# Optimization experiments

Measured on AMD Instinct MI355X. Metric: run time of the kernel, lower is better.

## Reference

```python
import jax, jax.numpy as jnp
import numpy as np

TAU = 2.0        # args.tau default (spikingjelly LIFNode)
V_TH = 1.0       # v_threshold
V_RESET = 0.0    # v_reset (hard reset)
ALPHA = 2.0      # ATan surrogate alpha

@jax.custom_vjp
def atan_spike(x):
    # Heaviside spike with ATan surrogate gradient (spikingjelly surrogate.ATan)
    return (x >= 0.0).astype(x.dtype)

def _atan_fwd(x):
    return atan_spike(x), x

def _atan_bwd(x, g):
    sg = (ALPHA / 2.0) / (1.0 + (jnp.pi / 2.0 * ALPHA * x) ** 2)
    return (g * sg,)

atan_spike.defvjp(_atan_fwd, _atan_bwd)

def setup_inputs() -> dict:
    key = jax.random.key(0)
    k1, k2, k3 = jax.random.split(key, 3)
    T, B, IN, OUT, NC = 16, 512, 3072, 2048, 10
    x_seq = jax.random.normal(k1, (T, B, IN), dtype=jnp.float32)
    # xavier-uniform-like scale: sqrt(2/(fan_in+fan_out))
    fc_w = jax.random.normal(k2, (OUT, IN), dtype=jnp.float32) * np.sqrt(2.0 / (IN + OUT)).astype(np.float32)
    fc_b = jnp.zeros((OUT,), jnp.float32)
    aux_w = jax.random.normal(k3, (NC, OUT), dtype=jnp.float32) * np.sqrt(2.0 / (OUT + NC)).astype(np.float32)
    aux_b = jnp.zeros((NC,), jnp.float32)
    return {"x_seq": x_seq, "fc_w": fc_w, "fc_b": fc_b, "aux_w": aux_w, "aux_b": aux_b}

def reference(x_seq, fc_w, fc_b, aux_w, aux_b):
    # fc over all timesteps: [T,B,in] @ [out,in]^T -> [T,B,out]
    cur_seq = jnp.einsum('tbi,oi->tbo', x_seq, fc_w) + fc_b

    def step(v, c):
        # LIF charge: v += (x - (v - v_reset)) / tau
        v = v + (c - (v - V_RESET)) / TAU
        s = atan_spike(v - V_TH)
        s_d = jax.lax.stop_gradient(s)  # detach_reset=True
        v = (1.0 - s_d) * v + s_d * V_RESET  # hard reset
        return v, s

    v0 = jnp.full(cur_seq.shape[1:], V_RESET, cur_seq.dtype)  # reset_net -> v = v_reset
    _, spk_seq = jax.lax.scan(step, v0, cur_seq)  # spk_seq: [T,B,out]
    count = spk_seq.sum(axis=0)                    # [B,out]
    logits = count @ aux_w.T + aux_b               # aux_head local logits [B,10]
    return spk_seq, count, logits
```

## Files before the change

kernel.cpp:

```cpp
#include <hip/hip_runtime.h>
#include <hip/hip_bf16.h>
#include <stdint.h>

#define T_   16
#define B_   512
#define IN_  3072
#define OUT_ 2048
#define NC_  10
#define M_   (T_ * B_)

#define BM 128
#define BN 128

#define SPK_SZ ((size_t)T_ * B_ * OUT_)
#define CNT_SZ ((size_t)B_ * OUT_)

#define TOL 4e-4
#define MAXFLAG (B_ * OUT_)

#define BK2   32
#define NCH2  (IN_ / BK2)
#define TILE_US 8192
#define APAN (M_ / BM)
#define BPAN (OUT_ / BN)

#define A_PREP_BLOCKS (APAN * NCH2 * 2)
#define B_PREP_BLOCKS (BPAN * NCH2 * 2)

typedef __attribute__((ext_vector_type(8))) short s16x8;
typedef __attribute__((ext_vector_type(4))) float f32x4;

__device__ unsigned int g_ctr;
__device__ unsigned int g_list[MAXFLAG];

__global__ void zero_ctr() { if (threadIdx.x == 0) g_ctr = 0; }

__device__ __forceinline__ unsigned short f2bf(float f) {
    __bf16 h = (__bf16)f;
    return *(unsigned short*)&h;
}
__device__ __forceinline__ float bf2f(unsigned short u) {
    union { unsigned int i; float f; } c; c.i = ((unsigned int)u) << 16; return c.f;
}
__device__ __forceinline__ int swz8(int r, int g) {
    return r * 64 + ((g ^ (r & 7)) << 3);
}

__device__ __forceinline__ void gload_lds16(const void* g, void* l) {
    __builtin_amdgcn_global_load_lds(
        (const __attribute__((address_space(1))) unsigned int*)g,
        (__attribute__((address_space(3))) unsigned int*)l, 16, 0, 0);
}

__global__ __launch_bounds__(256)
void prep2(const float* __restrict__ x, const float* __restrict__ w,
           unsigned short* __restrict__ Adig, unsigned short* __restrict__ Bdig)
{
    if (blockIdx.x == 0 && threadIdx.x == 0) g_ctr = 0;

    const float* src; unsigned short* dst; int id;
    if (blockIdx.x < A_PREP_BLOCKS) {
        src = x; dst = Adig; id = blockIdx.x * 256 + threadIdx.x;
    } else {
        src = w; dst = Bdig; id = (blockIdx.x - A_PREP_BLOCKS) * 256 + threadIdx.x;
    }
    const int gk = id & 3;
    const int r  = (id >> 2) & 127;
    const int ch = (id >> 9) % NCH2;
    const int pa = id / (NCH2 * 512);
    const int m  = pa * 128 + r;
    const int k  = ch * BK2 + gk * 8;

    float f[8];
    *(float4*)&f[0] = *(const float4*)(src + (size_t)m * IN_ + k);
    *(float4*)&f[4] = *(const float4*)(src + (size_t)m * IN_ + k + 4);
    s16x8 hi, lo;
#pragma unroll
    for (int j = 0; j < 8; ++j) {
        unsigned short hb = f2bf(f[j]);
        hi[j] = (short)hb;
        lo[j] = (short)f2bf(f[j] - bf2f(hb));
    }
    unsigned short* tb = dst + ((size_t)pa * NCH2 + ch) * TILE_US;
    *(s16x8*)&tb[swz8(r, gk)]     = hi;
    *(s16x8*)&tb[swz8(r, gk + 4)] = lo;
}

__global__ __launch_bounds__(256, 2)
void gemm_lds(const unsigned short* __restrict__ Adig,
              const unsigned short* __restrict__ Bdig,
              float* __restrict__ cur)
{
    __shared__ __align__(16) unsigned short Ash[2][TILE_US];
    __shared__ __align__(16) unsigned short Bsh[2][TILE_US];

    const int tid = threadIdx.x;
    const int l   = tid & 63;
    const int wv  = tid >> 6;
    const int wm  = (wv >> 1) * 64;
    const int wn  = (wv & 1) * 64;

    const int lin = blockIdx.x;
    const int xcd = lin & 7;
    const int jj  = lin >> 3;
    const int pm  = xcd * 8 + (jj & 7);
    const int pn  = jj >> 3;
    const int m0  = pm * BM;
    const int n0  = pn * BN;

    f32x4 acc[4][4];
#pragma unroll
    for (int i = 0; i < 4; ++i)
#pragma unroll
        for (int j = 0; j < 4; ++j) acc[i][j] = (f32x4)0.0f;

    const int lp = l & 15;
    const int lq = l >> 4;
    const int l8 = l * 8;

    const unsigned short* Abase = Adig + (size_t)pm * NCH2 * TILE_US;
    const unsigned short* Bbase = Bdig + (size_t)pn * NCH2 * TILE_US;

    auto stage = [&](int ch, int d) {
        if (wv < 2) {
            const unsigned short* sA = Abase + (size_t)ch * TILE_US + wv * 4096;
            unsigned short* dA = &Ash[d][wv * 4096];
#pragma unroll
            for (int i = 0; i < 8; ++i)
                gload_lds16(sA + i * 512 + l8, dA + i * 512);
        } else {
            const unsigned short* sB = Bbase + (size_t)ch * TILE_US + (wv - 2) * 4096;
            unsigned short* dB = &Bsh[d][(wv - 2) * 4096];
#pragma unroll
            for (int i = 0; i < 8; ++i)
                gload_lds16(sB + i * 512 + l8, dB + i * 512);
        }
    };

    stage(0, 0);

    for (int ch = 0; ch < NCH2; ++ch) {
        const int d = ch & 1;
        if (ch + 1 < NCH2) {
            stage(ch + 1, d ^ 1);
            asm volatile("s_waitcnt vmcnt(8)" ::: "memory");
        } else {
            asm volatile("s_waitcnt vmcnt(0)" ::: "memory");
        }
        __builtin_amdgcn_s_barrier();
        asm volatile("" ::: "memory");

        s16x8 a1f[4], a2f[4], b1f[4], b2f[4];
#pragma unroll
        for (int i = 0; i < 4; ++i) {
            const int ra = wm + i * 16 + lp;
            a1f[i] = *(const s16x8*)&Ash[d][swz8(ra, lq)];
            a2f[i] = *(const s16x8*)&Ash[d][swz8(ra, lq + 4)];
            const int rb = wn + i * 16 + lp;
            b1f[i] = *(const s16x8*)&Bsh[d][swz8(rb, lq)];
            b2f[i] = *(const s16x8*)&Bsh[d][swz8(rb, lq + 4)];
        }
        asm volatile("s_waitcnt lgkmcnt(0)" ::: "memory");
        __builtin_amdgcn_s_barrier();

        __builtin_amdgcn_s_setprio(1);
#pragma unroll
        for (int i = 0; i < 4; ++i)
#pragma unroll
            for (int j = 0; j < 4; ++j) {
                acc[i][j] = __builtin_amdgcn_mfma_f32_16x16x32_bf16(
                    a1f[i], b1f[j], acc[i][j], 0, 0, 0);
                acc[i][j] = __builtin_amdgcn_mfma_f32_16x16x32_bf16(
                    a2f[i], b1f[j], acc[i][j], 0, 0, 0);
                acc[i][j] = __builtin_amdgcn_mfma_f32_16x16x32_bf16(
                    a1f[i], b2f[j], acc[i][j], 0, 0, 0);
            }
        __builtin_amdgcn_s_setprio(0);
    }

    const int crow = lq * 4, ccol = lp;
#pragma unroll
    for (int i = 0; i < 4; ++i)
#pragma unroll
        for (int j = 0; j < 4; ++j) {
            const size_t mbase = (size_t)(m0 + wm + i * 16 + crow);
            const int o = n0 + wn + j * 16 + ccol;
#pragma unroll
            for (int reg = 0; reg < 4; ++reg)
                cur[(mbase + reg) * OUT_ + o] = acc[i][j][reg];
        }
}

__global__ __launch_bounds__(256, 2)
void gemm_split(const float* __restrict__ x, const float* __restrict__ w,
                float* __restrict__ cur)
{
    __shared__ __align__(16) unsigned short A1[BM * 64];
    __shared__ __align__(16) unsigned short A2[BM * 64];
    __shared__ __align__(16) unsigned short B1[BN * 64];
    __shared__ __align__(16) unsigned short B2[BN * 64];

    const int tid = threadIdx.x;
    const int l   = tid & 63;
    const int wv  = tid >> 6;
    const int wm  = (wv >> 1) * 64;
    const int wn  = (wv & 1) * 64;
    const int m0  = blockIdx.x * BM;
    const int n0  = blockIdx.y * BN;

    const int r = tid >> 1;
    const int h = tid & 1;
    const float* xa = x + (size_t)(m0 + r) * IN_ + h * 32;
    const float* wa = w + (size_t)(n0 + r) * IN_ + h * 32;

    f32x4 acc[4][4];
#pragma unroll
    for (int i = 0; i < 4; ++i)
#pragma unroll
        for (int j = 0; j < 4; ++j) acc[i][j] = (f32x4)0.0f;

    const int lp = l & 15;
    const int lq = l >> 4;

    for (int ch = 0; ch < 48; ++ch) {
        const int k0 = ch * 64;
        __syncthreads();
        float fx[32], fw[32];
#pragma unroll
        for (int i = 0; i < 8; ++i)
            *(float4*)&fx[4 * i] = *(const float4*)(xa + k0 + 4 * i);
#pragma unroll
        for (int i = 0; i < 8; ++i)
            *(float4*)&fw[4 * i] = *(const float4*)(wa + k0 + 4 * i);

#pragma unroll
        for (int q = 0; q < 4; ++q) {
            s16x8 vh, vl, uh, ul;
#pragma unroll
            for (int j = 0; j < 8; ++j) {
                float f = fx[8 * q + j];
                unsigned short hb = f2bf(f);
                vh[j] = (short)hb;
                vl[j] = (short)f2bf(f - bf2f(hb));
                float g = fw[8 * q + j];
                unsigned short gb = f2bf(g);
                uh[j] = (short)gb;
                ul[j] = (short)f2bf(g - bf2f(gb));
            }
            const int gg = h * 4 + q;
            *(s16x8*)&A1[swz8(r, gg)] = vh;
            *(s16x8*)&A2[swz8(r, gg)] = vl;
            *(s16x8*)&B1[swz8(r, gg)] = uh;
            *(s16x8*)&B2[swz8(r, gg)] = ul;
        }
        __syncthreads();

#pragma unroll
        for (int kk = 0; kk < 2; ++kk) {
            const int gb = kk * 4 + lq;
            s16x8 a1f[4], a2f[4], b1f[4], b2f[4];
#pragma unroll
            for (int i = 0; i < 4; ++i) {
                const int ra = wm + i * 16 + lp;
                a1f[i] = *(const s16x8*)&A1[swz8(ra, gb)];
                a2f[i] = *(const s16x8*)&A2[swz8(ra, gb)];
                const int rb = wn + i * 16 + lp;
                b1f[i] = *(const s16x8*)&B1[swz8(rb, gb)];
                b2f[i] = *(const s16x8*)&B2[swz8(rb, gb)];
            }
#pragma unroll
            for (int i = 0; i < 4; ++i)
#pragma unroll
                for (int j = 0; j < 4; ++j) {
                    acc[i][j] = __builtin_amdgcn_mfma_f32_16x16x32_bf16(
                        a1f[i], b1f[j], acc[i][j], 0, 0, 0);
                    acc[i][j] = __builtin_amdgcn_mfma_f32_16x16x32_bf16(
                        a2f[i], b1f[j], acc[i][j], 0, 0, 0);
                    acc[i][j] = __builtin_amdgcn_mfma_f32_16x16x32_bf16(
                        a1f[i], b2f[j], acc[i][j], 0, 0, 0);
                }
        }
    }

    const int crow = lq * 4, ccol = lp;
#pragma unroll
    for (int i = 0; i < 4; ++i)
#pragma unroll
        for (int j = 0; j < 4; ++j) {
            const size_t mbase = (size_t)(m0 + wm + i * 16 + crow);
            const int o = n0 + wn + j * 16 + ccol;
#pragma unroll
            for (int reg = 0; reg < 4; ++reg)
                cur[(mbase + reg) * OUT_ + o] = acc[i][j][reg];
        }
}

__global__ __launch_bounds__(256)
void lif_pass(const float* __restrict__ fcb, float* __restrict__ out)
{
    const int idx = blockIdx.x * 256 + threadIdx.x;
    const int o = idx & (OUT_ - 1);
    const double bias = (double)fcb[o];
    double v = 0.0; int cnt = 0; bool fl = false;
#pragma unroll
    for (int t = 0; t < T_; ++t) {
        const size_t p = (size_t)t * CNT_SZ + idx;
        double c = (double)out[p] + bias;
        v = v + (c - v) * 0.5;
        double d = v - 1.0;
        bool s = d >= 0.0;
        if (fabs(d) < TOL) fl = true;
        out[p] = s ? 1.0f : 0.0f;
        cnt += s ? 1 : 0;
        if (s) v = 0.0;
    }
    out[SPK_SZ + idx] = (float)cnt;
    if (fl) {
        unsigned int pI = atomicAdd(&g_ctr, 1u);
        g_list[pI] = (unsigned int)idx;
    }
}

__global__ void fixup(const float* __restrict__ x, const float* __restrict__ w,
                      const float* __restrict__ fcb, float* __restrict__ out)
{
    int nf = (int)g_ctr; if (nf > MAXFLAG) nf = MAXFLAG;
    const int lane = threadIdx.x & 63;
    const int wid  = (blockIdx.x * blockDim.x + threadIdx.x) >> 6;
    const int nw   = (gridDim.x * blockDim.x) >> 6;

    for (int i = wid; i < nf; i += nw) {
        unsigned int e = g_list[i];
        int b = (int)(e >> 11), o = (int)(e & (OUT_ - 1));
        double part[T_];
#pragma unroll
        for (int t = 0; t < T_; ++t) part[t] = 0.0;
        const float* wrow = w + (size_t)o * IN_;
        for (int k = lane; k < IN_; k += 64) {
            double wvv = (double)wrow[k];
#pragma unroll
            for (int t = 0; t < T_; ++t)
                part[t] = fma((double)x[((size_t)t * B_ + b) * IN_ + k], wvv, part[t]);
        }
#pragma unroll
        for (int t = 0; t < T_; ++t)
#pragma unroll
            for (int off = 32; off > 0; off >>= 1)
                part[t] += __shfl_xor(part[t], off, 64);
        if (lane == 0) {
            double bias = (double)fcb[o];
            double v = 0.0; int cnt = 0;
#pragma unroll
            for (int t = 0; t < T_; ++t) {
                double c = part[t] + bias;
                v = v + (c - v) * 0.5;
                bool s = (v - 1.0) >= 0.0;
                out[(size_t)t * CNT_SZ + (size_t)b * OUT_ + o] = s ? 1.0f : 0.0f;
                cnt += s ? 1 : 0;
                if (s) v = 0.0;
            }
            out[SPK_SZ + (size_t)b * OUT_ + o] = (float)cnt;
        }
    }
}

__global__ void aux_logits(const float* __restrict__ cnt,
                           const float* __restrict__ aw,
                           const float* __restrict__ ab,
                           float* __restrict__ lg)
{
    const int b = blockIdx.x;
    const int lane = threadIdx.x;
    double p0=0,p1=0,p2=0,p3=0,p4=0,p5=0,p6=0,p7=0,p8=0,p9=0;
    for (int o = lane; o < OUT_; o += 64) {
        double c = (double)cnt[(size_t)b * OUT_ + o];
        p0 = fma(c, (double)aw[0 * OUT_ + o], p0);
        p1 = fma(c, (double)aw[1 * OUT_ + o], p1);
        p2 = fma(c, (double)aw[2 * OUT_ + o], p2);
        p3 = fma(c, (double)aw[3 * OUT_ + o], p3);
        p4 = fma(c, (double)aw[4 * OUT_ + o], p4);
        p5 = fma(c, (double)aw[5 * OUT_ + o], p5);
        p6 = fma(c, (double)aw[6 * OUT_ + o], p6);
        p7 = fma(c, (double)aw[7 * OUT_ + o], p7);
        p8 = fma(c, (double)aw[8 * OUT_ + o], p8);
        p9 = fma(c, (double)aw[9 * OUT_ + o], p9);
    }
#pragma unroll
    for (int off = 32; off > 0; off >>= 1) {
        p0 += __shfl_xor(p0, off, 64); p1 += __shfl_xor(p1, off, 64);
        p2 += __shfl_xor(p2, off, 64); p3 += __shfl_xor(p3, off, 64);
        p4 += __shfl_xor(p4, off, 64); p5 += __shfl_xor(p5, off, 64);
        p6 += __shfl_xor(p6, off, 64); p7 += __shfl_xor(p7, off, 64);
        p8 += __shfl_xor(p8, off, 64); p9 += __shfl_xor(p9, off, 64);
    }
    if (lane == 0) {
        double pv[NC_] = {p0,p1,p2,p3,p4,p5,p6,p7,p8,p9};
#pragma unroll
        for (int c = 0; c < NC_; ++c)
            lg[(size_t)b * NC_ + c] = (float)(pv[c] + (double)ab[c]);
    }
}

extern "C" void kernel_launch(void* const* d_in, const int* in_sizes, int n_in,
                              void* d_out, int out_size, void* d_ws, size_t ws_size,
                              hipStream_t stream)
{
    (void)in_sizes; (void)n_in; (void)out_size;
    const float* x   = (const float*)d_in[0];
    const float* w   = (const float*)d_in[1];
    const float* fcb = (const float*)d_in[2];
    const float* aw  = (const float*)d_in[3];
    const float* ab  = (const float*)d_in[4];
    float* out = (float*)d_out;

    const size_t needA = (size_t)APAN * NCH2 * TILE_US * 2;
    const size_t needB = (size_t)BPAN * NCH2 * TILE_US * 2;

    if (ws_size >= needA + needB) {
        unsigned short* Adig = (unsigned short*)d_ws;
        unsigned short* Bdig = Adig + (size_t)APAN * NCH2 * TILE_US;
        prep2<<<dim3(A_PREP_BLOCKS + B_PREP_BLOCKS), dim3(256), 0, stream>>>(
            x, w, Adig, Bdig);
        gemm_lds<<<dim3(APAN * BPAN), dim3(256), 0, stream>>>(Adig, Bdig, out);
    } else {
        zero_ctr<<<dim3(1), dim3(64), 0, stream>>>();
        gemm_split<<<dim3(M_ / BM, OUT_ / BN), dim3(256), 0, stream>>>(x, w, out);
    }

    lif_pass<<<dim3(CNT_SZ / 256), dim3(256), 0, stream>>>(fcb, out);

    fixup<<<dim3(512), dim3(256), 0, stream>>>(x, w, fcb, out);

    aux_logits<<<dim3(B_), dim3(64), 0, stream>>>(
        out + SPK_SZ, aw, ab, out + SPK_SZ + CNT_SZ);
}
```

Baseline: 387.3 us.

## Fuse LIF scan into GEMM epilogue with time-interleaved A row layout

Reorders the A operand during prep so each 128-row GEMM tile holds all 16 timesteps for 8 batch rows. The GEMM epilogue stages the accumulators in shared memory and runs the LIF recurrence, spike writes, counts and near-threshold flagging in place. This drops the separate lif_pass kernel and the full write and re-read of the fp32 current tensor. It also tightens the near-threshold tolerance, which shrinks the fixup workload, and bounds-checks the flag list.

```diff
diff --git a/kernel.cpp b/kernel.cpp
--- a/kernel.cpp
+++ b/kernel.cpp
@@ -15,7 +15,7 @@
 #define SPK_SZ ((size_t)T_ * B_ * OUT_)
 #define CNT_SZ ((size_t)B_ * OUT_)
 
-#define TOL 4e-4
+#define TOL 2.5e-4
 #define MAXFLAG (B_ * OUT_)
 
 #define BK2   32
@@ -58,11 +58,11 @@
 {
     if (blockIdx.x == 0 && threadIdx.x == 0) g_ctr = 0;
 
-    const float* src; unsigned short* dst; int id;
+    const float* src; unsigned short* dst; int id; bool isA;
     if (blockIdx.x < A_PREP_BLOCKS) {
-        src = x; dst = Adig; id = blockIdx.x * 256 + threadIdx.x;
+        src = x; dst = Adig; id = blockIdx.x * 256 + threadIdx.x; isA = true;
     } else {
-        src = w; dst = Bdig; id = (blockIdx.x - A_PREP_BLOCKS) * 256 + threadIdx.x;
+        src = w; dst = Bdig; id = (blockIdx.x - A_PREP_BLOCKS) * 256 + threadIdx.x; isA = false;
     }
     const int gk = id & 3;
     const int r  = (id >> 2) & 127;
@@ -71,9 +71,13 @@
     const int m  = pa * 128 + r;
     const int k  = ch * BK2 + gk * 8;
 
+    size_t srow;
+    if (isA) srow = (size_t)(m & 15) * B_ + (m >> 4);
+    else     srow = (size_t)m;
+
     float f[8];
-    *(float4*)&f[0] = *(const float4*)(src + (size_t)m * IN_ + k);
-    *(float4*)&f[4] = *(const float4*)(src + (size_t)m * IN_ + k + 4);
+    *(float4*)&f[0] = *(const float4*)(src + srow * IN_ + k);
+    *(float4*)&f[4] = *(const float4*)(src + srow * IN_ + k + 4);
     s16x8 hi, lo;
 #pragma unroll
     for (int j = 0; j < 8; ++j) {
@@ -87,12 +91,14 @@
 }
 
 __global__ __launch_bounds__(256, 2)
-void gemm_lds(const unsigned short* __restrict__ Adig,
-              const unsigned short* __restrict__ Bdig,
-              float* __restrict__ cur)
-{
-    __shared__ __align__(16) unsigned short Ash[2][TILE_US];
-    __shared__ __align__(16) unsigned short Bsh[2][TILE_US];
+void gemm_fused(const unsigned short* __restrict__ Adig,
+                const unsigned short* __restrict__ Bdig,
+                const float* __restrict__ fcb,
+                float* __restrict__ out)
+{
+    __shared__ __align__(16) unsigned short SH[4 * TILE_US];
+    unsigned short* Ash0 = SH;
+    unsigned short* Bsh0 = SH + 2 * TILE_US;
 
     const int tid = threadIdx.x;
     const int l   = tid & 63;
@@ -105,7 +111,6 @@
     const int jj  = lin >> 3;
     const int pm  = xcd * 8 + (jj & 7);
     const int pn  = jj >> 3;
-    const int m0  = pm * BM;
     const int n0  = pn * BN;
 
     f32x4 acc[4][4];
@@ -124,13 +129,13 @@
     auto stage = [&](int ch, int d) {
         if (wv < 2) {
             const unsigned short* sA = Abase + (size_t)ch * TILE_US + wv * 4096;
-            unsigned short* dA = &Ash[d][wv * 4096];
+            unsigned short* dA = Ash0 + d * TILE_US + wv * 4096;
 #pragma unroll
             for (int i = 0; i < 8; ++i)
                 gload_lds16(sA + i * 512 + l8, dA + i * 512);
         } else {
             const unsigned short* sB = Bbase + (size_t)ch * TILE_US + (wv - 2) * 4096;
-            unsigned short* dB = &Bsh[d][(wv - 2) * 4096];
+            unsigned short* dB = Bsh0 + d * TILE_US + (wv - 2) * 4096;
 #pragma unroll
             for (int i = 0; i < 8; ++i)
                 gload_lds16(sB + i * 512 + l8, dB + i * 512);
@@ -154,11 +159,11 @@
 #pragma unroll
         for (int i = 0; i < 4; ++i) {
             const int ra = wm + i * 16 + lp;
-            a1f[i] = *(const s16x8*)&Ash[d][swz8(ra, lq)];
-            a2f[i] = *(const s16x8*)&Ash[d][swz8(ra, lq + 4)];
+            a1f[i] = *(const s16x8*)&Ash0[d * TILE_US + swz8(ra, lq)];
+            a2f[i] = *(const s16x8*)&Ash0[d * TILE_US + swz8(ra, lq + 4)];
             const int rb = wn + i * 16 + lp;
-            b1f[i] = *(const s16x8*)&Bsh[d][swz8(rb, lq)];
-            b2f[i] = *(const s16x8*)&Bsh[d][swz8(rb, lq + 4)];
+            b1f[i] = *(const s16x8*)&Bsh0[d * TILE_US + swz8(rb, lq)];
+            b2f[i] = *(const s16x8*)&Bsh0[d * TILE_US + swz8(rb, lq + 4)];
         }
         asm volatile("s_waitcnt lgkmcnt(0)" ::: "memory");
         __builtin_amdgcn_s_barrier();
@@ -178,17 +183,51 @@
         __builtin_amdgcn_s_setprio(0);
     }
 
-    const int crow = lq * 4, ccol = lp;
+    __syncthreads();
+    float* cf = (float*)SH;
+
+    const int crow0 = lq * 4;
 #pragma unroll
     for (int i = 0; i < 4; ++i)
 #pragma unroll
-        for (int j = 0; j < 4; ++j) {
-            const size_t mbase = (size_t)(m0 + wm + i * 16 + crow);
-            const int o = n0 + wn + j * 16 + ccol;
-#pragma unroll
-            for (int reg = 0; reg < 4; ++reg)
-                cur[(mbase + reg) * OUT_ + o] = acc[i][j][reg];
-        }
+        for (int j = 0; j < 4; ++j)
+#pragma unroll
+            for (int reg = 0; reg < 4; ++reg) {
+                const int row = wm + i * 16 + crow0 + reg;
+                const int col = wn + j * 16 + lp;
+                cf[row * 128 + (col ^ ((row & 7) << 2))] = acc[i][j][reg];
+            }
+    __syncthreads();
+
+    const int o_l = tid & 127;
+    const int o   = n0 + o_l;
+    const double bias = (double)fcb[o];
+    const int bq0 = (tid >> 7) * 4;
+
+#pragma unroll
+    for (int q = 0; q < 4; ++q) {
+        const int bl = bq0 + q;
+        const int b  = pm * 8 + bl;
+        double v = 0.0; int cnt = 0; bool fl = false;
+#pragma unroll
+        for (int t = 0; t < T_; ++t) {
+            const int row = bl * 16 + t;
+            const float c32 = cf[row * 128 + (o_l ^ ((row & 7) << 2))];
+            const double c = (double)c32 + bias;
+            v = v + (c - v) * 0.5;
+            const double dlt = v - 1.0;
+            const bool s = dlt >= 0.0;
+            if (fabs(dlt) < TOL) fl = true;
+            out[(size_t)t * CNT_SZ + (size_t)b * OUT_ + o] = s ? 1.0f : 0.0f;
+            cnt += s ? 1 : 0;
+            if (s) v = 0.0;
+        }
+        out[SPK_SZ + (size_t)b * OUT_ + o] = (float)cnt;
+        if (fl) {
+            unsigned int idx = atomicAdd(&g_ctr, 1u);
+            if (idx < MAXFLAG) g_list[idx] = (unsigned int)(b * OUT_ + o);
+        }
+    }
 }
 
 __global__ __launch_bounds__(256, 2)
@@ -317,7 +356,7 @@
     out[SPK_SZ + idx] = (float)cnt;
     if (fl) {
         unsigned int pI = atomicAdd(&g_ctr, 1u);
-        g_list[pI] = (unsigned int)idx;
+        if (pI < MAXFLAG) g_list[pI] = (unsigned int)idx;
     }
 }
 
@@ -421,13 +460,12 @@
         unsigned short* Bdig = Adig + (size_t)APAN * NCH2 * TILE_US;
         prep2<<<dim3(A_PREP_BLOCKS + B_PREP_BLOCKS), dim3(256), 0, stream>>>(
             x, w, Adig, Bdig);
-        gemm_lds<<<dim3(APAN * BPAN), dim3(256), 0, stream>>>(Adig, Bdig, out);
+        gemm_fused<<<dim3(APAN * BPAN), dim3(256), 0, stream>>>(Adig, Bdig, fcb, out);
     } else {
         zero_ctr<<<dim3(1), dim3(64), 0, stream>>>();
         gemm_split<<<dim3(M_ / BM, OUT_ / BN), dim3(256), 0, stream>>>(x, w, out);
-    }
-
-    lif_pass<<<dim3(CNT_SZ / 256), dim3(256), 0, stream>>>(fcb, out);
+        lif_pass<<<dim3(CNT_SZ / 256), dim3(256), 0, stream>>>(fcb, out);
+    }
 
     fixup<<<dim3(512), dim3(256), 0, stream>>>(x, w, fcb, out);
 
```

New measurement: 360.6 us. 6.9% less time.
